# Kernel tuning notes

Measured on AMD Instinct MI355X. Metric: run time of the kernel, lower is better.

## Reference

```python
import jax, jax.numpy as jnp
import numpy as np

NUM_EXPERTS = 64
D_MODEL = 1024
D_FF = 2048
TOKENS_PER_EXPERT = 512
TOTAL_TOKENS = NUM_EXPERTS * TOKENS_PER_EXPERT  # 32768


def setup_inputs() -> dict:
    key = jax.random.key(0)
    k_in, k_w1, k_w2 = jax.random.split(key, 3)
    inputs = jax.random.normal(k_in, (TOTAL_TOKENS, D_MODEL), dtype=jnp.float32)
    # Per-expert FFN weights: w1 [E, d_model, d_ff], w2 [E, d_ff, d_model]
    s1 = 1.0 / np.sqrt(D_MODEL)
    s2 = 1.0 / np.sqrt(D_FF)
    w1 = jax.random.normal(k_w1, (NUM_EXPERTS, D_MODEL, D_FF), dtype=jnp.float32) * s1
    w2 = jax.random.normal(k_w2, (NUM_EXPERTS, D_FF, D_MODEL), dtype=jnp.float32) * s2
    return {"inputs": inputs, "w1": w1, "w2": w2}


def reference(inputs, w1, w2):
    # Equal-size chunk dispatch (split_size_or_sections=None):
    # inputs.chunk(E, dim=0) -> per-expert blocks of TOKENS_PER_EXPERT rows.
    E = w1.shape[0]
    x = inputs.reshape(E, -1, inputs.shape[-1])          # [E, C, d_model]
    # Grouped FFN: expert e applies Linear -> GELU -> Linear to its chunk.
    h = jax.nn.gelu(jnp.einsum('ecd,edf->ecf', x, w1))   # [E, C, d_ff]
    y = jnp.einsum('ecf,efd->ecd', h, w2)                # [E, C, d_model]
    # torch.cat along split_dim=0
    return y.reshape(-1, inputs.shape[-1])               # [T, d_model]
```

## Files before the change

kernel.cpp:

```cpp
#include <hip/hip_runtime.h>
#include <hip/hip_bf16.h>
#include <cstdint>
#include <cstddef>

constexpr int NE  = 64;
constexpr int DM  = 1024;
constexpr int DF  = 2048;
constexpr int CPE = 512;

typedef float  f32x4  __attribute__((ext_vector_type(4)));
typedef short  bf16x8 __attribute__((ext_vector_type(8)));

__device__ __forceinline__ short f2bf(float f) {
    union { __hip_bfloat16 h; short s; } u;
    u.h = __float2bfloat16(f);
    return u.s;
}

__device__ __forceinline__ float gelu_tanh(float x) {
    float z = 0.7978845608028654f * (x + 0.044715f * x * x * x);
    float e = __expf(2.0f * z);
    float t = 1.0f - 2.0f / (e + 1.0f);
    return 0.5f * x * (1.0f + t);
}

template <int KTOT, int NTOT, bool GELU_OUT, bool A_BF16>
__global__ __launch_bounds__(256)
void ffn_gemm(const void* __restrict__ Ag, const float* __restrict__ Bg, void* __restrict__ Cg)
{
    constexpr int BPE = (NTOT / 128) * 4;
    const int bid = blockIdx.x;
    const int e   = bid / BPE;
    const int t   = bid % BPE;
    const int mt  = t & 3;
    const int nt  = t >> 2;

    __shared__ short As[128 * 40];
    __shared__ short Bs[128 * 40];

    const int tid  = threadIdx.x;
    const int lane = tid & 63;
    const int wave = tid >> 6;
    const int wm   = wave & 1;
    const int wn   = wave >> 1;

    const int am = tid >> 1;
    const int ak = (tid & 1) << 4;
    const int bn = (tid & 63) << 1;
    const int bk = (tid >> 6) << 3;

    const size_t arow0 = (size_t)(e * CPE + mt * 128);
    const float* Bge = Bg + (size_t)e * KTOT * NTOT + nt * 128;

    f32x4 acc[4][4];
#pragma unroll
    for (int i = 0; i < 4; ++i)
#pragma unroll
        for (int j = 0; j < 4; ++j) acc[i][j] = f32x4{0.f, 0.f, 0.f, 0.f};

    const int fr = lane & 15;
    const int fq = (lane >> 4) << 3;

    for (int kk = 0; kk < KTOT; kk += 32) {
        if constexpr (A_BF16) {
            const short* Ab = (const short*)Ag + (arow0 + am) * (size_t)KTOT + kk + ak;
            uint4 v0 = *(const uint4*)(Ab);
            uint4 v1 = *(const uint4*)(Ab + 8);
            *(uint4*)&As[am * 40 + ak]     = v0;
            *(uint4*)&As[am * 40 + ak + 8] = v1;
        } else {
            const float* Af = (const float*)Ag + (arow0 + am) * (size_t)KTOT + kk + ak;
            float4 v0 = *(const float4*)(Af + 0);
            float4 v1 = *(const float4*)(Af + 4);
            float4 v2 = *(const float4*)(Af + 8);
            float4 v3 = *(const float4*)(Af + 12);
            bf16x8 s0, s1;
            s0[0]=f2bf(v0.x); s0[1]=f2bf(v0.y); s0[2]=f2bf(v0.z); s0[3]=f2bf(v0.w);
            s0[4]=f2bf(v1.x); s0[5]=f2bf(v1.y); s0[6]=f2bf(v1.z); s0[7]=f2bf(v1.w);
            s1[0]=f2bf(v2.x); s1[1]=f2bf(v2.y); s1[2]=f2bf(v2.z); s1[3]=f2bf(v2.w);
            s1[4]=f2bf(v3.x); s1[5]=f2bf(v3.y); s1[6]=f2bf(v3.z); s1[7]=f2bf(v3.w);
            *(bf16x8*)&As[am * 40 + ak]     = s0;
            *(bf16x8*)&As[am * 40 + ak + 8] = s1;
        }
        {
            const float* pb = Bge + (size_t)(kk + bk) * NTOT + bn;
            float2 bv[8];
#pragma unroll
            for (int j = 0; j < 8; ++j) bv[j] = *(const float2*)(pb + (size_t)j * NTOT);
            bf16x8 s0, s1;
#pragma unroll
            for (int j = 0; j < 8; ++j) { s0[j] = f2bf(bv[j].x); s1[j] = f2bf(bv[j].y); }
            *(bf16x8*)&Bs[(bn + 0) * 40 + bk] = s0;
            *(bf16x8*)&Bs[(bn + 1) * 40 + bk] = s1;
        }
        __syncthreads();

        bf16x8 af[4], bf[4];
#pragma unroll
        for (int i = 0; i < 4; ++i)
            af[i] = *(const bf16x8*)&As[(wm * 64 + i * 16 + fr) * 40 + fq];
#pragma unroll
        for (int j = 0; j < 4; ++j)
            bf[j] = *(const bf16x8*)&Bs[(wn * 64 + j * 16 + fr) * 40 + fq];
#pragma unroll
        for (int i = 0; i < 4; ++i)
#pragma unroll
            for (int j = 0; j < 4; ++j)
                acc[i][j] = __builtin_amdgcn_mfma_f32_16x16x32_bf16(af[i], bf[j], acc[i][j], 0, 0, 0);
        __syncthreads();
    }

    const int lr = (lane >> 4) << 2;
    const int lc = lane & 15;
    const size_t crow0 = arow0 + wm * 64;
    const int    ccol0 = nt * 128 + wn * 64;
#pragma unroll
    for (int i = 0; i < 4; ++i) {
#pragma unroll
        for (int r = 0; r < 4; ++r) {
            const size_t row = crow0 + i * 16 + lr + r;
#pragma unroll
            for (int j = 0; j < 4; ++j) {
                float v = acc[i][j][r];
                const size_t idx = row * (size_t)NTOT + ccol0 + j * 16 + lc;
                if constexpr (GELU_OUT) {
                    ((__hip_bfloat16*)Cg)[idx] = __float2bfloat16(gelu_tanh(v));
                } else {
                    ((float*)Cg)[idx] = v;
                }
            }
        }
    }
}

extern "C" void kernel_launch(void* const* d_in, const int* in_sizes, int n_in,
                              void* d_out, int out_size, void* d_ws, size_t ws_size,
                              hipStream_t stream)
{
    const float* X  = (const float*)d_in[0];
    const float* W1 = (const float*)d_in[1];
    const float* W2 = (const float*)d_in[2];
    float*       Y  = (float*)d_out;

    __hip_bfloat16* H = (__hip_bfloat16*)d_ws;

    ffn_gemm<DM, DF, true, false><<<dim3(NE * 64), dim3(256), 0, stream>>>(
        (const void*)X, W1, (void*)H);

    ffn_gemm<DF, DM, false, true><<<dim3(NE * 32), dim3(256), 0, stream>>>(
        (const void*)H, W2, (void*)Y);
}
```

Baseline: 1.581 ms.

## Pre-cast inputs and pre-transpose weights to bf16, use direct-to-LDS loads

Adds separate pre-pass kernels that cast X to bf16 and transpose-cast W1/W2 to bf16 K-major layout in workspace. A new GEMM then loads both operands through global_load_lds with a BK=64 tile, so the main loop no longer does per-tile fp32 conversion or strided weight loads. It pays extra passes over the weights and activations and needs a large workspace; the old path is kept as a fallback when the workspace is too small. W2t reuses the Xb region after the first GEMM.

```diff
diff --git a/kernel.cpp b/kernel.cpp
--- a/kernel.cpp
+++ b/kernel.cpp
@@ -22,6 +22,148 @@
     float e = __expf(2.0f * z);
     float t = 1.0f - 2.0f / (e + 1.0f);
     return 0.5f * x * (1.0f + t);
+}
+
+__device__ __forceinline__ void gld_lds16(const short* g, short* l) {
+    __builtin_amdgcn_global_load_lds((const __attribute__((address_space(1))) void*)g,
+                                     (__attribute__((address_space(3))) void*)l,
+                                     16, 0, 0);
+}
+
+
+__global__ __launch_bounds__(256) void conv_cast(const float* __restrict__ X,
+                                                 short* __restrict__ Xb) {
+    size_t i = (size_t)blockIdx.x * 256 + threadIdx.x;
+    const float4* p = (const float4*)X + 2 * i;
+    float4 a = p[0], b = p[1];
+    bf16x8 s;
+    s[0] = f2bf(a.x); s[1] = f2bf(a.y); s[2] = f2bf(a.z); s[3] = f2bf(a.w);
+    s[4] = f2bf(b.x); s[5] = f2bf(b.y); s[6] = f2bf(b.z); s[7] = f2bf(b.w);
+    ((bf16x8*)Xb)[i] = s;
+}
+
+template <int K, int N>
+__global__ __launch_bounds__(256) void conv_transpose(const float* __restrict__ W,
+                                                      short* __restrict__ WT) {
+    constexpr int KT = K / 64, NT = N / 64;
+    const int bid = blockIdx.x;
+    const int e  = bid / (KT * NT);
+    const int t  = bid % (KT * NT);
+    const int k0 = (t % KT) * 64;
+    const int n0 = (t / KT) * 64;
+
+    __shared__ short tile[64 * 72];
+
+    const float* src = W + ((size_t)e * K + k0) * (size_t)N + n0;
+    const int tc = (threadIdx.x & 15) * 4;
+    const int tr = threadIdx.x >> 4;
+#pragma unroll
+    for (int p = 0; p < 4; ++p) {
+        const int r = p * 16 + tr;
+        float4 v = *(const float4*)(src + (size_t)r * N + tc);
+        tile[(tc + 0) * 72 + r] = f2bf(v.x);
+        tile[(tc + 1) * 72 + r] = f2bf(v.y);
+        tile[(tc + 2) * 72 + r] = f2bf(v.z);
+        tile[(tc + 3) * 72 + r] = f2bf(v.w);
+    }
+    __syncthreads();
+    short* dst = WT + ((size_t)e * N + n0) * (size_t)K + k0;
+    const int wk = (threadIdx.x & 7) * 8;
+    const int wn = threadIdx.x >> 3;
+#pragma unroll
+    for (int p = 0; p < 2; ++p) {
+        const int n = p * 32 + wn;
+        *(uint4*)(dst + (size_t)n * K + wk) = *(const uint4*)&tile[n * 72 + wk];
+    }
+}
+
+template <int KTOT, int NTOT, bool GELU_OUT>
+__global__ __launch_bounds__(256)
+void gemm_bt(const short* __restrict__ A, const short* __restrict__ BT,
+             void* __restrict__ C) {
+    constexpr int NT = NTOT / 128;
+    const int bid = blockIdx.x;
+    const int e  = bid / (4 * NT);
+    const int t  = bid % (4 * NT);
+    const int mt = t & 3;
+    const int nt = t >> 2;
+
+    __shared__ short As[8192];
+    __shared__ short Bs[8192];
+
+    const int tid = threadIdx.x, lane = tid & 63, w = tid >> 6;
+    const int wm = w & 1, wn = w >> 1;
+
+    const size_t arow0 = (size_t)e * CPE + (size_t)mt * 128;
+    const short* Ae = A + arow0 * KTOT;
+    const short* Be = BT + ((size_t)e * NTOT + (size_t)nt * 128) * KTOT;
+
+    f32x4 acc[4][4];
+#pragma unroll
+    for (int i = 0; i < 4; ++i)
+#pragma unroll
+        for (int j = 0; j < 4; ++j) acc[i][j] = f32x4{0.f, 0.f, 0.f, 0.f};
+
+    const int fr = lane & 15;
+    const int fq = (lane >> 4) << 3;
+
+    int rowS[4], colS[4];
+#pragma unroll
+    for (int i = 0; i < 4; ++i) {
+        const int L = (w * 4 + i) * 512 + lane * 8;
+        const int panel = L >> 12;
+        const int rm = L & 4095;
+        rowS[i] = rm >> 5;
+        colS[i] = (panel << 5) + (L & 31);
+    }
+
+    for (int kk = 0; kk < KTOT; kk += 64) {
+#pragma unroll
+        for (int i = 0; i < 4; ++i) {
+            const int c = w * 4 + i;
+            gld_lds16(Ae + (size_t)rowS[i] * KTOT + kk + colS[i], As + c * 512);
+            gld_lds16(Be + (size_t)rowS[i] * KTOT + kk + colS[i], Bs + c * 512);
+        }
+        __syncthreads();
+#pragma unroll
+        for (int p = 0; p < 2; ++p) {
+            bf16x8 af[4], bfr[4];
+#pragma unroll
+            for (int i = 0; i < 4; ++i)
+                af[i] = *(const bf16x8*)&As[p * 4096 + (wm * 64 + i * 16 + fr) * 32 + fq];
+#pragma unroll
+            for (int j = 0; j < 4; ++j)
+                bfr[j] = *(const bf16x8*)&Bs[p * 4096 + (wn * 64 + j * 16 + fr) * 32 + fq];
+#pragma unroll
+            for (int i = 0; i < 4; ++i)
+#pragma unroll
+                for (int j = 0; j < 4; ++j)
+                    acc[i][j] = __builtin_amdgcn_mfma_f32_16x16x32_bf16(af[i], bfr[j], acc[i][j], 0, 0, 0);
+        }
+        __syncthreads();
+    }
+
+    const int lr = (lane >> 4) << 2;
+    const int lc = lane & 15;
+    const size_t crow0 = arow0 + (size_t)wm * 64;
+    const int    ccol0 = nt * 128 + wn * 64;
+#pragma unroll
+    for (int i = 0; i < 4; ++i) {
+#pragma unroll
+        for (int r = 0; r < 4; ++r) {
+            const size_t row = crow0 + i * 16 + lr + r;
+#pragma unroll
+            for (int j = 0; j < 4; ++j) {
+                float v = acc[i][j][r];
+                const size_t idx = row * (size_t)NTOT + ccol0 + j * 16 + lc;
+                if constexpr (GELU_OUT) {
+                    ((short*)C)[idx] = f2bf(gelu_tanh(v));
+                } else {
+                    ((float*)C)[idx] = v;
+                }
+            }
+        }
+    }
 }
 
 template <int KTOT, int NTOT, bool GELU_OUT, bool A_BF16>
@@ -95,18 +237,18 @@
         }
         __syncthreads();
 
-        bf16x8 af[4], bf[4];
+        bf16x8 af[4], bfr[4];
 #pragma unroll
         for (int i = 0; i < 4; ++i)
             af[i] = *(const bf16x8*)&As[(wm * 64 + i * 16 + fr) * 40 + fq];
 #pragma unroll
         for (int j = 0; j < 4; ++j)
-            bf[j] = *(const bf16x8*)&Bs[(wn * 64 + j * 16 + fr) * 40 + fq];
+            bfr[j] = *(const bf16x8*)&Bs[(wn * 64 + j * 16 + fr) * 40 + fq];
 #pragma unroll
         for (int i = 0; i < 4; ++i)
 #pragma unroll
             for (int j = 0; j < 4; ++j)
-                acc[i][j] = __builtin_amdgcn_mfma_f32_16x16x32_bf16(af[i], bf[j], acc[i][j], 0, 0, 0);
+                acc[i][j] = __builtin_amdgcn_mfma_f32_16x16x32_bf16(af[i], bfr[j], acc[i][j], 0, 0, 0);
         __syncthreads();
     }
 
@@ -137,16 +279,31 @@
                               void* d_out, int out_size, void* d_ws, size_t ws_size,
                               hipStream_t stream)
 {
+    (void)in_sizes; (void)n_in; (void)out_size;
     const float* X  = (const float*)d_in[0];
     const float* W1 = (const float*)d_in[1];
     const float* W2 = (const float*)d_in[2];
     float*       Y  = (float*)d_out;
 
-    __hip_bfloat16* H = (__hip_bfloat16*)d_ws;
-
-    ffn_gemm<DM, DF, true, false><<<dim3(NE * 64), dim3(256), 0, stream>>>(
-        (const void*)X, W1, (void*)H);
-
-    ffn_gemm<DF, DM, false, true><<<dim3(NE * 32), dim3(256), 0, stream>>>(
-        (const void*)H, W2, (void*)Y);
-}
+    const size_t XB_B  = (size_t)NE * CPE * DM * 2;
+    const size_t W1T_B = (size_t)NE * DM * DF * 2;
+    const size_t H_B   = (size_t)NE * CPE * DF * 2;
+    const size_t REQ   = XB_B + W1T_B + H_B;
+
+    if (ws_size >= REQ) {
+        short* Xb  = (short*)d_ws;
+        short* W1t = (short*)((char*)d_ws + XB_B);
+        short* W2t = (short*)d_ws;
+        short* H   = (short*)((char*)d_ws + XB_B + W1T_B);
+
+        conv_cast<<<dim3((NE * CPE * DM) / (8 * 256)), dim3(256), 0, stream>>>(X, Xb);
+        conv_transpose<DM, DF><<<dim3(NE * (DM / 64) * (DF / 64)), dim3(256), 0, stream>>>(W1, W1t);
+        gemm_bt<DM, DF, true><<<dim3(NE * 4 * (DF / 128)), dim3(256), 0, stream>>>(Xb, W1t, (void*)H);
+        conv_transpose<DF, DM><<<dim3(NE * (DF / 64) * (DM / 64)), dim3(256), 0, stream>>>(W2, W2t);
+        gemm_bt<DF, DM, false><<<dim3(NE * 4 * (DM / 128)), dim3(256), 0, stream>>>(H, W2t, (void*)Y);
+    } else {
+        __hip_bfloat16* H = (__hip_bfloat16*)d_ws;
+        ffn_gemm<DM, DF, true,  false><<<dim3(NE * 64), dim3(256), 0, stream>>>((const void*)X, W1, (void*)H);
+        ffn_gemm<DF, DM, false, true ><<<dim3(NE * 32), dim3(256), 0, stream>>>((const void*)H, W2, (void*)Y);
+    }
+}
```

After: 1.582 ms. Within noise of the previous version (+0.0%).
